# Kernel tuning notes

Measured on AMD Instinct MI355X. Metric: run time of the kernel, lower is better.

Reference implementation:

```python
import jax, jax.numpy as jnp
import numpy as np

MEM = 2048

def _linear_params(key, scale):
    kw, kb = jax.random.split(key)
    W = jax.random.uniform(kw, (MEM, MEM), jnp.float32, -scale, scale)
    b = jax.random.uniform(kb, (MEM,), jnp.float32, -scale, scale)
    return W, b

def setup_inputs() -> dict:
    key = jax.random.key(0)
    ks = jax.random.split(key, 18)
    scale = 1.0 / np.sqrt(MEM)
    inp = {
        'lc': jax.random.normal(ks[0], (1, MEM), jnp.float32),
        'lh': jax.random.normal(ks[1], (1, MEM), jnp.float32),
        'rc': jax.random.normal(ks[2], (1, MEM), jnp.float32),
        'rh': jax.random.normal(ks[3], (1, MEM), jnp.float32),
        'S': jax.random.normal(ks[4], (1, MEM), jnp.float32),
        'w': jax.random.normal(ks[5], (1, MEM), jnp.float32),
    }
    names = ['Wh', 'Us', 'ma', 'ilh', 'irh', 'lflh', 'lfrh', 'rflh', 'rfrh', 'ulh', 'urh']
    for i, n in enumerate(names):
        W, b = _linear_params(ks[6 + i], scale)
        inp[n + '_w'] = W
        inp[n + '_b'] = b
    return inp

def _lin(x, W, b):
    return x @ W.T + b

def reference(lc, lh, rc, rh, S, w,
              Wh_w, Wh_b, Us_w, Us_b, ma_w, ma_b,
              ilh_w, ilh_b, irh_w, irh_b,
              lflh_w, lflh_b, lfrh_w, lfrh_b,
              rflh_w, rflh_b, rfrh_w, rfrh_b,
              ulh_w, ulh_b, urh_w, urh_b):
    # attention scoring over the two children
    m_left = jnp.tanh(_lin(lh, Wh_w, Wh_b) + _lin(S, Us_w, Us_b)).squeeze()   # [MEM]
    m_right = jnp.tanh(_lin(rh, Wh_w, Wh_b) + _lin(S, Us_w, Us_b)).squeeze()  # [MEM]
    exp_left = w @ m_left[:, None]    # [1,1]
    exp_right = w @ m_right[:, None]  # [1,1]
    denom = exp_left + exp_right
    left_alpha = exp_left / denom
    right_alpha = exp_right / denom
    # attention-weighted child hidden states
    la = jnp.tanh(_lin(left_alpha * lh, ma_w, ma_b))   # [1,MEM]
    ra = jnp.tanh(_lin(right_alpha * rh, ma_w, ma_b))  # [1,MEM]
    # tree-LSTM gates
    i = jax.nn.sigmoid(_lin(la, ilh_w, ilh_b) + _lin(ra, irh_w, irh_b))
    lf = jax.nn.sigmoid(_lin(la, lflh_w, lflh_b) + _lin(ra, lfrh_w, lfrh_b))
    rf = jax.nn.sigmoid(_lin(la, rflh_w, rflh_b) + _lin(ra, rfrh_w, rfrh_b))
    update = jnp.tanh(_lin(la, ulh_w, ulh_b) + _lin(ra, urh_w, urh_b))
    c = i * update + lf * lc + rf * rc
    h = jnp.tanh(c)
    return (c, h)
```

## Files before the change

### kernel.cpp

```cpp
#include <hip/hip_runtime.h>
#include <math.h>

#define MEM  2048
#define NT   256
#define NT1  192

struct Params {
    const float *lc, *rc, *lh, *rh, *S, *w;
    const float *Wh_w, *Wh_b, *Us_w, *Us_b, *ma_w, *ma_b;
    const float *ilh_w, *ilh_b, *irh_w, *irh_b;
    const float *lflh_w, *lflh_b, *lfrh_w, *lfrh_b;
    const float *rflh_w, *rflh_b, *rfrh_w, *rfrh_b;
    const float *ulh_w, *ulh_b, *urh_w, *urh_b;
    float *pl, *pr, *wml, *wmr, *out;
};

__device__ __forceinline__ float dot4(float4 a, float4 b) {
    return a.x * b.x + a.y * b.y + a.z * b.z + a.w * b.w;
}

__device__ __forceinline__ float wave_reduce(float v) {
#pragma unroll
    for (int off = 32; off > 0; off >>= 1)
        v += __shfl_down(v, off, 64);
    return v;
}

__device__ __forceinline__ float tanh_fast(float x) {
    x = fminf(15.0f, fmaxf(-15.0f, x));
    const float e = __expf(2.0f * x);
    return (e - 1.0f) / (e + 1.0f);
}
__device__ __forceinline__ float sigmoid_fast(float x) {
    return 1.0f / (1.0f + __expf(-x));
}

__global__ __launch_bounds__(NT1, 2) void k1(Params p)
{
    __shared__ float s_par[5];

    const int t   = threadIdx.x;
    const int wv  = t >> 6, ln = t & 63;
    const int row = blockIdx.x;

    const float4* l4 = (const float4*)p.lh;
    const float4* r4 = (const float4*)p.rh;
    const float4* s4 = (const float4*)p.S;

    if (wv == 0) {
        const float4* w4 = (const float4*)(p.Wh_w + (size_t)row * MEM);
        float4 wb[8];
#pragma unroll
        for (int j = 0; j < 8; ++j) wb[j] = w4[ln + 64 * j];
        float awl = 0.f, awr = 0.f;
#pragma unroll
        for (int j = 0; j < 8; ++j) {
            awl += dot4(wb[j], l4[ln + 64 * j]);
            awr += dot4(wb[j], r4[ln + 64 * j]);
        }
        awl = wave_reduce(awl);
        awr = wave_reduce(awr);
        if (ln == 0) { s_par[0] = awl; s_par[1] = awr; }
    } else if (wv == 1) {
        const float4* u4 = (const float4*)(p.Us_w + (size_t)row * MEM);
        float4 ub[8];
#pragma unroll
        for (int j = 0; j < 8; ++j) ub[j] = u4[ln + 64 * j];
        float aus = 0.f;
#pragma unroll
        for (int j = 0; j < 8; ++j)
            aus += dot4(ub[j], s4[ln + 64 * j]);
        aus = wave_reduce(aus);
        if (ln == 0) s_par[2] = aus;
    } else {
        const float4* m4 = (const float4*)(p.ma_w + (size_t)row * MEM);
        float4 mb[8];
#pragma unroll
        for (int j = 0; j < 8; ++j) mb[j] = m4[ln + 64 * j];
        float aml = 0.f, amr = 0.f;
#pragma unroll
        for (int j = 0; j < 8; ++j) {
            aml += dot4(mb[j], l4[ln + 64 * j]);
            amr += dot4(mb[j], r4[ln + 64 * j]);
        }
        aml = wave_reduce(aml);
        amr = wave_reduce(amr);
        if (ln == 0) { s_par[3] = aml; s_par[4] = amr; }
    }
    __syncthreads();

    if (t == 0) {
        const float us  = s_par[2] + p.Us_b[row];
        const float whb = p.Wh_b[row];
        const float ml  = tanh_fast(s_par[0] + whb + us);
        const float mr  = tanh_fast(s_par[1] + whb + us);
        p.pl[row] = s_par[3];
        p.pr[row] = s_par[4];
        const float wj = p.w[row];
        p.wml[row] = wj * ml;
        p.wmr[row] = wj * mr;
    }
}

__global__ __launch_bounds__(NT) void kmid(Params p)
{
    __shared__ float s_red[4][2];
    __shared__ float s_al[2];

    const int t  = threadIdx.x;
    const int wv = t >> 6, ln = t & 63;

    const float4* wl4 = (const float4*)p.wml;
    const float4* wr4 = (const float4*)p.wmr;
    const float4 a0 = wl4[t], a1 = wl4[t + NT];
    const float4 b0 = wr4[t], b1 = wr4[t + NT];
    float el = a0.x + a0.y + a0.z + a0.w + a1.x + a1.y + a1.z + a1.w;
    float er = b0.x + b0.y + b0.z + b0.w + b1.x + b1.y + b1.z + b1.w;
    el = wave_reduce(el);
    er = wave_reduce(er);
    if (ln == 0) { s_red[wv][0] = el; s_red[wv][1] = er; }
    __syncthreads();
    if (t == 0) {
        const float e0 = s_red[0][0] + s_red[1][0] + s_red[2][0] + s_red[3][0];
        const float e1 = s_red[0][1] + s_red[1][1] + s_red[2][1] + s_red[3][1];
        const float d  = e0 + e1;
        s_al[0] = e0 / d;
        s_al[1] = e1 / d;
    }
    __syncthreads();
    const float al = s_al[0];
    const float ar = s_al[1];

    const float4* p4 = (const float4*)p.pl;
    const float4* q4 = (const float4*)p.pr;
    const float4* b4 = (const float4*)p.ma_b;
    float4* xa4 = (float4*)p.wml;
    float4* xb4 = (float4*)p.wmr;
#pragma unroll
    for (int h = 0; h < 2; ++h) {
        const int i = t + h * NT;
        const float4 pp = p4[i];
        const float4 qq = q4[i];
        const float4 bb = b4[i];
        float4 xa, xb;
        xa.x = tanh_fast(al * pp.x + bb.x); xb.x = tanh_fast(ar * qq.x + bb.x);
        xa.y = tanh_fast(al * pp.y + bb.y); xb.y = tanh_fast(ar * qq.y + bb.y);
        xa.z = tanh_fast(al * pp.z + bb.z); xb.z = tanh_fast(ar * qq.z + bb.z);
        xa.w = tanh_fast(al * pp.w + bb.w); xb.w = tanh_fast(ar * qq.w + bb.w);
        xa4[i] = xa;
        xb4[i] = xb;
    }
}

__global__ __launch_bounds__(NT, 2) void k2(Params p)
{
    __shared__ float s_g[4];

    const int t   = threadIdx.x;
    const int wv  = t >> 6, ln = t & 63;
    const int row = blockIdx.x;

    const float bI  = p.ilh_b[row]  + p.irh_b[row];
    const float bLF = p.lflh_b[row] + p.lfrh_b[row];
    const float bRF = p.rflh_b[row] + p.rfrh_b[row];
    const float bU  = p.ulh_b[row]  + p.urh_b[row];
    const float lcv = p.lc[row], rcv = p.rc[row];

    const float *wlp, *wrp;
    if      (wv == 0) { wlp = p.ilh_w;  wrp = p.irh_w;  }
    else if (wv == 1) { wlp = p.lflh_w; wrp = p.lfrh_w; }
    else if (wv == 2) { wlp = p.rflh_w; wrp = p.rfrh_w; }
    else              { wlp = p.ulh_w;  wrp = p.urh_w;  }

    const float4* wl4  = (const float4*)(wlp + (size_t)row * MEM);
    const float4* wr4  = (const float4*)(wrp + (size_t)row * MEM);
    const float4* xag4 = (const float4*)p.wml;
    const float4* xbg4 = (const float4*)p.wmr;

    float4 ab[8], bb[8];
#pragma unroll
    for (int j = 0; j < 8; ++j) ab[j] = wl4[ln + 64 * j];
#pragma unroll
    for (int j = 0; j < 8; ++j) bb[j] = wr4[ln + 64 * j];

    float accA = 0.f, accB = 0.f;
#pragma unroll
    for (int j = 0; j < 8; ++j) accA += dot4(ab[j], xag4[ln + 64 * j]);
#pragma unroll
    for (int j = 0; j < 8; ++j) accB += dot4(bb[j], xbg4[ln + 64 * j]);

    const float g = wave_reduce(accA + accB);
    if (ln == 0) s_g[wv] = g;
    __syncthreads();

    if (t == 0) {
        const float ig  = sigmoid_fast(s_g[0] + bI);
        const float lfg = sigmoid_fast(s_g[1] + bLF);
        const float rfg = sigmoid_fast(s_g[2] + bRF);
        const float ug  = tanh_fast(s_g[3] + bU);
        const float c   = ig * ug + lfg * lcv + rfg * rcv;
        p.out[row]       = c;
        p.out[MEM + row] = tanh_fast(c);
    }
}

extern "C" void kernel_launch(void* const* d_in, const int* in_sizes, int n_in,
                              void* d_out, int out_size, void* d_ws, size_t ws_size,
                              hipStream_t stream)
{
    Params h;
    h.lc = (const float*)d_in[0];
    h.lh = (const float*)d_in[1];
    h.rc = (const float*)d_in[2];
    h.rh = (const float*)d_in[3];
    h.S  = (const float*)d_in[4];
    h.w  = (const float*)d_in[5];
    h.Wh_w   = (const float*)d_in[6];   h.Wh_b   = (const float*)d_in[7];
    h.Us_w   = (const float*)d_in[8];   h.Us_b   = (const float*)d_in[9];
    h.ma_w   = (const float*)d_in[10];  h.ma_b   = (const float*)d_in[11];
    h.ilh_w  = (const float*)d_in[12];  h.ilh_b  = (const float*)d_in[13];
    h.irh_w  = (const float*)d_in[14];  h.irh_b  = (const float*)d_in[15];
    h.lflh_w = (const float*)d_in[16];  h.lflh_b = (const float*)d_in[17];
    h.lfrh_w = (const float*)d_in[18];  h.lfrh_b = (const float*)d_in[19];
    h.rflh_w = (const float*)d_in[20];  h.rflh_b = (const float*)d_in[21];
    h.rfrh_w = (const float*)d_in[22];  h.rfrh_b = (const float*)d_in[23];
    h.ulh_w  = (const float*)d_in[24];  h.ulh_b  = (const float*)d_in[25];
    h.urh_w  = (const float*)d_in[26];  h.urh_b  = (const float*)d_in[27];

    float* ws = (float*)d_ws;
    h.pl  = ws;
    h.pr  = ws + MEM;
    h.wml = ws + 2 * MEM;
    h.wmr = ws + 3 * MEM;
    h.out = (float*)d_out;

    k1  <<<MEM, NT1, 0, stream>>>(h);
    kmid<<<1,   NT,  0, stream>>>(h);
    k2  <<<MEM, NT,  0, stream>>>(h);
}
```

Before: 242.8 us.

## Issue weight loads via inline asm and stage input vectors in LDS

Both matrix-vector kernels now issue all weight-row loads up front with inline global_load_dwordx4 asm, so the compiler cannot reorder or split them. The activation vectors are copied cooperatively into shared memory and read from LDS during the dot products, instead of each wave reading them from global memory. Launch bounds are raised to 4 blocks per CU to allow more blocks in flight. Each block now does an extra vector copy into LDS plus a barrier, and uses 24KB (k1) or 16KB (k2) of shared memory, which may limit occupancy.

```diff
diff --git a/kernel.cpp b/kernel.cpp
--- a/kernel.cpp
+++ b/kernel.cpp
@@ -2,8 +2,15 @@
 #include <math.h>
 
 #define MEM  2048
+#define NF4  (MEM / 4)
 #define NT   256
 #define NT1  192
+
+typedef float vf4 __attribute__((ext_vector_type(4)));
+
+#define GLOAD(dst, ptr, OFF) \
+    asm volatile("global_load_dwordx4 %0, %1, off offset:" #OFF \
+                 : "=v"(dst) : "v"(ptr) : "memory")
 
 struct Params {
     const float *lc, *rc, *lh, *rh, *S, *w;
@@ -15,8 +22,8 @@
     float *pl, *pr, *wml, *wmr, *out;
 };
 
-__device__ __forceinline__ float dot4(float4 a, float4 b) {
-    return a.x * b.x + a.y * b.y + a.z * b.z + a.w * b.w;
+__device__ __forceinline__ float dotv(vf4 a, float4 b) {
+    return a[0] * b.x + a[1] * b.y + a[2] * b.z + a[3] * b.w;
 }
 
 __device__ __forceinline__ float wave_reduce(float v) {
@@ -35,54 +42,83 @@
     return 1.0f / (1.0f + __expf(-x));
 }
 
-__global__ __launch_bounds__(NT1, 2) void k1(Params p)
+__global__ __launch_bounds__(NT1, 4) void k1(Params p)
 {
+    __shared__ __align__(16) float s_l[MEM];
+    __shared__ __align__(16) float s_r[MEM];
+    __shared__ __align__(16) float s_s[MEM];
     __shared__ float s_par[5];
 
     const int t   = threadIdx.x;
     const int wv  = t >> 6, ln = t & 63;
     const int row = blockIdx.x;
 
-    const float4* l4 = (const float4*)p.lh;
-    const float4* r4 = (const float4*)p.rh;
-    const float4* s4 = (const float4*)p.S;
+    const float* mat = (wv == 0) ? p.Wh_w : (wv == 1) ? p.Us_w : p.ma_w;
+    const float* pa  = mat + (size_t)row * MEM + 4 * ln;
+    const float* pa2 = pa + 1024;
+
+    vf4 m0, m1, m2, m3, m4, m5, m6, m7;
+    GLOAD(m0, pa,  0);    GLOAD(m1, pa,  1024);
+    GLOAD(m2, pa,  2048); GLOAD(m3, pa,  3072);
+    GLOAD(m4, pa2, 0);    GLOAD(m5, pa2, 1024);
+    GLOAD(m6, pa2, 2048); GLOAD(m7, pa2, 3072);
+
+    {
+        const float4* l4g = (const float4*)p.lh;
+        const float4* r4g = (const float4*)p.rh;
+        const float4* s4g = (const float4*)p.S;
+        float4* sl = (float4*)s_l;
+        float4* sr = (float4*)s_r;
+        float4* ss = (float4*)s_s;
+        for (int i = t; i < NF4; i += NT1) {
+            sl[i] = l4g[i];
+            sr[i] = r4g[i];
+            ss[i] = s4g[i];
+        }
+    }
+    asm volatile("s_waitcnt vmcnt(0)" ::: "memory");
+    __builtin_amdgcn_sched_barrier(0);
+    __syncthreads();
+
+    const float4* sl4 = (const float4*)s_l;
+    const float4* sr4 = (const float4*)s_r;
+    const float4* ss4 = (const float4*)s_s;
 
     if (wv == 0) {
-        const float4* w4 = (const float4*)(p.Wh_w + (size_t)row * MEM);
-        float4 wb[8];
-#pragma unroll
-        for (int j = 0; j < 8; ++j) wb[j] = w4[ln + 64 * j];
         float awl = 0.f, awr = 0.f;
-#pragma unroll
-        for (int j = 0; j < 8; ++j) {
-            awl += dot4(wb[j], l4[ln + 64 * j]);
-            awr += dot4(wb[j], r4[ln + 64 * j]);
-        }
+        awl += dotv(m0, sl4[ln +   0]); awr += dotv(m0, sr4[ln +   0]);
+        awl += dotv(m1, sl4[ln +  64]); awr += dotv(m1, sr4[ln +  64]);
+        awl += dotv(m2, sl4[ln + 128]); awr += dotv(m2, sr4[ln + 128]);
+        awl += dotv(m3, sl4[ln + 192]); awr += dotv(m3, sr4[ln + 192]);
+        awl += dotv(m4, sl4[ln + 256]); awr += dotv(m4, sr4[ln + 256]);
+        awl += dotv(m5, sl4[ln + 320]); awr += dotv(m5, sr4[ln + 320]);
+        awl += dotv(m6, sl4[ln + 384]); awr += dotv(m6, sr4[ln + 384]);
+        awl += dotv(m7, sl4[ln + 448]); awr += dotv(m7, sr4[ln + 448]);
         awl = wave_reduce(awl);
         awr = wave_reduce(awr);
         if (ln == 0) { s_par[0] = awl; s_par[1] = awr; }
     } else if (wv == 1) {
-        const float4* u4 = (const float4*)(p.Us_w + (size_t)row * MEM);
-        float4 ub[8];
-#pragma unroll
-        for (int j = 0; j < 8; ++j) ub[j] = u4[ln + 64 * j];
         float aus = 0.f;
-#pragma unroll
-        for (int j = 0; j < 8; ++j)
-            aus += dot4(ub[j], s4[ln + 64 * j]);
+        aus += dotv(m0, ss4[ln +   0]);
+        aus += dotv(m1, ss4[ln +  64]);
+        aus += dotv(m2, ss4[ln + 128]);
+        aus += dotv(m3, ss4[ln + 192]);
+        aus += dotv(m4, ss4[ln + 256]);
+        aus += dotv(m5, ss4[ln + 320]);
+        aus += dotv(m6, ss4[ln + 384]);
+        aus += dotv(m7, ss4[ln + 448]);
         aus = wave_reduce(aus);
         if (ln == 0) s_par[2] = aus;
     } else {
-        const float4* m4 = (const float4*)(p.ma_w + (size_t)row * MEM);
-        float4 mb[8];
-#pragma unroll
-        for (int j = 0; j < 8; ++j) mb[j] = m4[ln + 64 * j];
         float aml = 0.f, amr = 0.f;
-#pragma unroll
-        for (int j = 0; j < 8; ++j) {
-            aml += dot4(mb[j], l4[ln + 64 * j]);
-            amr += dot4(mb[j], r4[ln + 64 * j]);
-        }
+        aml += dotv(m0, sl4[ln +   0]); amr += dotv(m0, sr4[ln +   0]);
+        aml += dotv(m1, sl4[ln +  64]); amr += dotv(m1, sr4[ln +  64]);
+        aml += dotv(m2, sl4[ln + 128]); amr += dotv(m2, sr4[ln + 128]);
+        aml += dotv(m3, sl4[ln + 192]); amr += dotv(m3, sr4[ln + 192]);
+        aml += dotv(m4, sl4[ln + 256]); amr += dotv(m4, sr4[ln + 256]);
+        aml += dotv(m5, sl4[ln + 320]); amr += dotv(m5, sr4[ln + 320]);
+        aml += dotv(m6, sl4[ln + 384]); amr += dotv(m6, sr4[ln + 384]);
+        aml += dotv(m7, sl4[ln + 448]); amr += dotv(m7, sr4[ln + 448]);
         aml = wave_reduce(aml);
         amr = wave_reduce(amr);
         if (ln == 0) { s_par[3] = aml; s_par[4] = amr; }
@@ -152,8 +188,10 @@
     }
 }
 
-__global__ __launch_bounds__(NT, 2) void k2(Params p)
+__global__ __launch_bounds__(NT, 4) void k2(Params p)
 {
+    __shared__ __align__(16) float s_xa[MEM];
+    __shared__ __align__(16) float s_xb[MEM];
     __shared__ float s_g[4];
 
     const int t   = threadIdx.x;
@@ -172,22 +210,48 @@
     else if (wv == 2) { wlp = p.rflh_w; wrp = p.rfrh_w; }
     else              { wlp = p.ulh_w;  wrp = p.urh_w;  }
 
-    const float4* wl4  = (const float4*)(wlp + (size_t)row * MEM);
-    const float4* wr4  = (const float4*)(wrp + (size_t)row * MEM);
-    const float4* xag4 = (const float4*)p.wml;
-    const float4* xbg4 = (const float4*)p.wmr;
-
-    float4 ab[8], bb[8];
-#pragma unroll
-    for (int j = 0; j < 8; ++j) ab[j] = wl4[ln + 64 * j];
-#pragma unroll
-    for (int j = 0; j < 8; ++j) bb[j] = wr4[ln + 64 * j];
+    const float* pa  = wlp + (size_t)row * MEM + 4 * ln;
+    const float* pb  = wrp + (size_t)row * MEM + 4 * ln;
+    const float* pa2 = pa + 1024;
+    const float* pb2 = pb + 1024;
+
+    vf4 a0, a1, a2, a3, a4, a5, a6, a7;
+    vf4 b0, b1, b2, b3, b4, b5, b6, b7;
+    GLOAD(a0, pa,  0);    GLOAD(a1, pa,  1024);
+    GLOAD(a2, pa,  2048); GLOAD(a3, pa,  3072);
+    GLOAD(a4, pa2, 0);    GLOAD(a5, pa2, 1024);
+    GLOAD(a6, pa2, 2048); GLOAD(a7, pa2, 3072);
+    GLOAD(b0, pb,  0);    GLOAD(b1, pb,  1024);
+    GLOAD(b2, pb,  2048); GLOAD(b3, pb,  3072);
+    GLOAD(b4, pb2, 0);    GLOAD(b5, pb2, 1024);
+    GLOAD(b6, pb2, 2048); GLOAD(b7, pb2, 3072);
+
+    {
+        const float4* xag4 = (const float4*)p.wml;
+        const float4* xbg4 = (const float4*)p.wmr;
+        float4* sa = (float4*)s_xa;
+        float4* sb = (float4*)s_xb;
+        sa[t]      = xag4[t];
+        sa[t + NT] = xag4[t + NT];
+        sb[t]      = xbg4[t];
+        sb[t + NT] = xbg4[t + NT];
+    }
+    asm volatile("s_waitcnt vmcnt(0)" ::: "memory");
+    __builtin_amdgcn_sched_barrier(0);
+    __syncthreads();
+
+    const float4* xa4 = (const float4*)s_xa;
+    const float4* xb4 = (const float4*)s_xb;
 
     float accA = 0.f, accB = 0.f;
-#pragma unroll
-    for (int j = 0; j < 8; ++j) accA += dot4(ab[j], xag4[ln + 64 * j]);
-#pragma unroll
-    for (int j = 0; j < 8; ++j) accB += dot4(bb[j], xbg4[ln + 64 * j]);
+    accA += dotv(a0, xa4[ln +   0]);  accB += dotv(b0, xb4[ln +   0]);
+    accA += dotv(a1, xa4[ln +  64]);  accB += dotv(b1, xb4[ln +  64]);
+    accA += dotv(a2, xa4[ln + 128]);  accB += dotv(b2, xb4[ln + 128]);
+    accA += dotv(a3, xa4[ln + 192]);  accB += dotv(b3, xb4[ln + 192]);
+    accA += dotv(a4, xa4[ln + 256]);  accB += dotv(b4, xb4[ln + 256]);
+    accA += dotv(a5, xa4[ln + 320]);  accB += dotv(b5, xb4[ln + 320]);
+    accA += dotv(a6, xa4[ln + 384]);  accB += dotv(b6, xb4[ln + 384]);
+    accA += dotv(a7, xa4[ln + 448]);  accB += dotv(b7, xb4[ln + 448]);
 
     const float g = wave_reduce(accA + accB);
     if (ln == 0) s_g[wv] = g;
```

Result: no change. 246.0 us (+1.3%).
